# Kernel tuning notes

Hardware: AMD Instinct MI355X
Metric: run time of the kernel (lower is better)

Reference implementation:

```python
import jax, jax.numpy as jnp
import numpy as np

B, S, H, NH = 2, 2048, 1024, 16
HD = H // NH  # 64


def setup_inputs() -> dict:
    key = jax.random.key(0)
    ks = jax.random.split(key, 9)
    w = lambda k: jax.random.normal(k, (H, H), dtype=jnp.float32) * 0.02  # torch Linear weight [out,in]
    b = lambda k: jax.random.normal(k, (H,), dtype=jnp.float32) * 0.02
    return {
        "hidden_states": jax.random.normal(ks[0], (B, S, H), dtype=jnp.float32),
        "Wq": w(ks[1]), "bq": b(ks[2]),
        "Wk": w(ks[3]), "bk": b(ks[4]),
        "Wv": w(ks[5]), "bv": b(ks[6]),
        "Wo": w(ks[7]), "bo": b(ks[8]),
    }


def reference(hidden_states, Wq, bq, Wk, bk, Wv, bv, Wo, bo):
    b, s, h = hidden_states.shape
    nh, hd = NH, h // NH

    def proj(W, bias):
        y = hidden_states @ W.T + bias  # torch Linear: x W^T + b
        return y.reshape(b, s, nh, hd).transpose(0, 2, 1, 3)  # [b, h, s, d]

    q = proj(Wq, bq)
    k = proj(Wk, bk)
    v = proj(Wv, bv)

    scale = jnp.sqrt(jnp.asarray(hd, dtype=q.dtype))
    scores = jnp.einsum("bhqd,bhkd->bhqk", q, k) / scale  # [b, h, s, s]
    pos = jnp.arange(s)
    causal = pos[:, None] < pos[None, :]  # True where masked (key after query)
    scores = jnp.where(causal[None, None], -jnp.inf, scores)
    attn = jax.nn.softmax(scores, axis=-1)
    out = jnp.einsum("bhqk,bhkd->bhqd", attn, v)
    out = out.transpose(0, 2, 1, 3).reshape(b, s, h)
    return out @ Wo.T + bo
```

## Files before the change

kernel.cpp:

```cpp
#include <hip/hip_runtime.h>
#include <stdint.h>

typedef __bf16 bf16;
typedef __attribute__((ext_vector_type(2))) __bf16 bf16x2;
typedef __attribute__((ext_vector_type(4))) __bf16 bf16x4;
typedef __attribute__((ext_vector_type(8))) __bf16 bf16x8;
typedef __attribute__((ext_vector_type(4))) float f32x4;
typedef __attribute__((ext_vector_type(4))) short s16x4;

#define B_  2
#define S_  2048
#define H_  1024
#define NH_ 16
#define HD_ 64

__device__ __forceinline__ void glds16(const bf16* g, bf16* l) {
  __builtin_amdgcn_global_load_lds(
      (const __attribute__((address_space(1))) uint32_t*)g,
      (__attribute__((address_space(3))) uint32_t*)l, 16, 0, 0);
}

__device__ __forceinline__ f32x4 pv_mfma(bf16x4 a, bf16x4 b, f32x4 c) {
#if __has_builtin(__builtin_amdgcn_mfma_f32_16x16x16bf16_1k)
  union U { bf16x4 h; s16x4 s; };
  U ua; ua.h = a;
  U ub; ub.h = b;
  return __builtin_amdgcn_mfma_f32_16x16x16bf16_1k(ua.s, ub.s, c, 0, 0, 0);
#else
  f32x4 d;
  asm volatile("v_mfma_f32_16x16x16_bf16 %0, %1, %2, %3\n\ts_nop 7\n\ts_nop 7"
               : "=v"(d) : "v"(a), "v"(b), "v"(c));
  return d;
#endif
}

__global__ __launch_bounds__(256) void cvt_f32_bf16(
    const float* __restrict__ s0, bf16* __restrict__ d0, int n0,
    const float* __restrict__ s1, bf16* __restrict__ d1,
    const float* __restrict__ s2, bf16* __restrict__ d2,
    const float* __restrict__ s3, bf16* __restrict__ d3,
    const float* __restrict__ s4, bf16* __restrict__ d4, int nw)
{
  const float* s; bf16* d; int n;
  switch (blockIdx.y) {
    case 0:  s = s0; d = d0; n = n0; break;
    case 1:  s = s1; d = d1; n = nw; break;
    case 2:  s = s2; d = d2; n = nw; break;
    case 3:  s = s3; d = d3; n = nw; break;
    default: s = s4; d = d4; n = nw; break;
  }
  const int i = (blockIdx.x * 256 + threadIdx.x) * 8;
  if (i >= n) return;
  float4 v0 = *(const float4*)(s + i);
  float4 v1 = *(const float4*)(s + i + 4);
  bf16x8 o;
  o[0] = (bf16)v0.x; o[1] = (bf16)v0.y; o[2] = (bf16)v0.z; o[3] = (bf16)v0.w;
  o[4] = (bf16)v1.x; o[5] = (bf16)v1.y; o[6] = (bf16)v1.z; o[7] = (bf16)v1.w;
  *(bf16x8*)(d + i) = o;
}

__global__ __launch_bounds__(256) void gemm_qkv(
    const bf16* __restrict__ X,
    const bf16* __restrict__ W0, const bf16* __restrict__ W1, const bf16* __restrict__ W2,
    const float* __restrict__ b0, const float* __restrict__ b1, const float* __restrict__ b2,
    bf16* __restrict__ Y0, bf16* __restrict__ Y1, bf16* __restrict__ Y2,
    float ys0, int M, int N, int K)
{
  const bf16* W; const float* bias; bf16* Y; float ysc;
  if (blockIdx.z == 0)      { W = W0; bias = b0; Y = Y0; ysc = ys0; }
  else if (blockIdx.z == 1) { W = W1; bias = b1; Y = Y1; ysc = 1.0f; }
  else                      { W = W2; bias = b2; Y = Y2; ysc = 1.0f; }

  __shared__ __align__(16) bf16 As[2][128 * 32];
  __shared__ __align__(16) bf16 Bs[2][128 * 32];

  const int tid  = threadIdx.x;
  const int lane = tid & 63;
  const int wave = tid >> 6;
  const int m0 = blockIdx.y * 128;
  const int n0 = blockIdx.x * 128;
  const int wm = (wave >> 1) * 64;
  const int wn = (wave & 1) * 64;

  const int r0 = tid >> 2,            c0 = (tid & 3) * 8;
  const int r1 = (256 + tid) >> 2,    c1 = ((256 + tid) & 3) * 8;
  const int cb0 = (wave * 64) * 8;
  const int cb1 = (256 + wave * 64) * 8;

  f32x4 acc[4][4] = {};

  glds16(X + (size_t)(m0 + r0) * K + c0, &As[0][cb0]);
  glds16(W + (size_t)(n0 + r0) * K + c0, &Bs[0][cb0]);
  glds16(X + (size_t)(m0 + r1) * K + c1, &As[0][cb1]);
  glds16(W + (size_t)(n0 + r1) * K + c1, &Bs[0][cb1]);

  int pb = 0;
  for (int k0 = 0; k0 < K; k0 += 32, pb ^= 1) {
    __syncthreads();

    if (k0 + 32 < K) {
      const int kn = k0 + 32;
      glds16(X + (size_t)(m0 + r0) * K + kn + c0, &As[pb ^ 1][cb0]);
      glds16(W + (size_t)(n0 + r0) * K + kn + c0, &Bs[pb ^ 1][cb0]);
      glds16(X + (size_t)(m0 + r1) * K + kn + c1, &As[pb ^ 1][cb1]);
      glds16(W + (size_t)(n0 + r1) * K + kn + c1, &Bs[pb ^ 1][cb1]);
    }

    bf16x8 a[4], b[4];
#pragma unroll
    for (int i = 0; i < 4; ++i)
      a[i] = *(const bf16x8*)&As[pb][(wm + i * 16 + (lane & 15)) * 32 + (lane >> 4) * 8];
#pragma unroll
    for (int i = 0; i < 4; ++i)
      b[i] = *(const bf16x8*)&Bs[pb][(wn + i * 16 + (lane & 15)) * 32 + (lane >> 4) * 8];
#pragma unroll
    for (int mi = 0; mi < 4; ++mi)
#pragma unroll
      for (int ni = 0; ni < 4; ++ni)
        acc[mi][ni] = __builtin_amdgcn_mfma_f32_16x16x32_bf16(a[mi], b[ni], acc[mi][ni], 0, 0, 0);
  }

#pragma unroll
  for (int mi = 0; mi < 4; ++mi) {
    const int row = m0 + wm + mi * 16 + (lane >> 4) * 4;
#pragma unroll
    for (int ni = 0; ni < 4; ++ni) {
      const int col = n0 + wn + ni * 16 + (lane & 15);
      const float bv = bias[col];
#pragma unroll
      for (int r = 0; r < 4; ++r)
        Y[(size_t)(row + r) * N + col] = (bf16)((acc[mi][ni][r] + bv) * ysc);
    }
  }
}

__global__ __launch_bounds__(256) void gemm_o_64(
    const bf16* __restrict__ X, const bf16* __restrict__ W,
    const float* __restrict__ bias, float* __restrict__ Y)
{
  constexpr int K = 1024, N = 1024;
  __shared__ __align__(16) bf16 As[2][64 * 32];
  __shared__ __align__(16) bf16 Bs[2][128 * 32];

  const int tid  = threadIdx.x;
  const int lane = tid & 63;
  const int wave = tid >> 6;
  const int m0 = blockIdx.y * 64;
  const int n0 = blockIdx.x * 128;
  const int wm = (wave >> 1) * 32;
  const int wn = (wave & 1) * 64;

  const int ar = tid >> 2,  ac = (tid & 3) * 8;
  const int br0 = tid >> 2,          bc0 = (tid & 3) * 8;
  const int br1 = (256 + tid) >> 2,  bc1 = ((256 + tid) & 3) * 8;
  const int acb  = (wave * 64) * 8;
  const int bcb0 = (wave * 64) * 8;
  const int bcb1 = (256 + wave * 64) * 8;

  f32x4 acc[2][4] = {};

  glds16(X + (size_t)(m0 + ar) * K + ac,   &As[0][acb]);
  glds16(W + (size_t)(n0 + br0) * K + bc0, &Bs[0][bcb0]);
  glds16(W + (size_t)(n0 + br1) * K + bc1, &Bs[0][bcb1]);

  int pb = 0;
  for (int k0 = 0; k0 < K; k0 += 32, pb ^= 1) {
    __syncthreads();

    if (k0 + 32 < K) {
      const int kn = k0 + 32;
      glds16(X + (size_t)(m0 + ar) * K + kn + ac,   &As[pb ^ 1][acb]);
      glds16(W + (size_t)(n0 + br0) * K + kn + bc0, &Bs[pb ^ 1][bcb0]);
      glds16(W + (size_t)(n0 + br1) * K + kn + bc1, &Bs[pb ^ 1][bcb1]);
    }

    bf16x8 a[2], b[4];
#pragma unroll
    for (int i = 0; i < 2; ++i)
      a[i] = *(const bf16x8*)&As[pb][(wm + i * 16 + (lane & 15)) * 32 + (lane >> 4) * 8];
#pragma unroll
    for (int i = 0; i < 4; ++i)
      b[i] = *(const bf16x8*)&Bs[pb][(wn + i * 16 + (lane & 15)) * 32 + (lane >> 4) * 8];
#pragma unroll
    for (int mi = 0; mi < 2; ++mi)
#pragma unroll
      for (int ni = 0; ni < 4; ++ni)
        acc[mi][ni] = __builtin_amdgcn_mfma_f32_16x16x32_bf16(a[mi], b[ni], acc[mi][ni], 0, 0, 0);
  }

#pragma unroll
  for (int mi = 0; mi < 2; ++mi) {
    const int row = m0 + wm + mi * 16 + (lane >> 4) * 4;
#pragma unroll
    for (int ni = 0; ni < 4; ++ni) {
      const int col = n0 + wn + ni * 16 + (lane & 15);
      const float bv = bias[col];
#pragma unroll
      for (int r = 0; r < 4; ++r)
        Y[(size_t)(row + r) * N + col] = acc[mi][ni][r] + bv;
    }
  }
}


#define STAGE_K(k0_, buf_)                                                  \
  {                                                                         \
    _Pragma("unroll")                                                       \
    for (int j = 0; j < 4; ++j) {                                           \
      const int n = j * 256 + tid;                                          \
      const int row = n >> 3;                                               \
      const int cg  = (n & 7) ^ (row & 7);                                  \
      glds16(Kp + (size_t)((k0_) + row) * H_ + cg * 8,                      \
             &Ks[buf_][(j * 256 + wave * 64) * 8]);                         \
    }                                                                       \
  }

#define LOAD_V(k0_)                                                         \
  {                                                                         \
    vreg[0] = *(const bf16x8*)(Vp + (size_t)((k0_) + vr) * H_ + vc);        \
    vreg[1] = *(const bf16x8*)(Vp + (size_t)((k0_) + vr) * H_ + vc + 8);    \
    vreg[2] = *(const bf16x8*)(Vp + (size_t)((k0_) + vr + 1) * H_ + vc);    \
    vreg[3] = *(const bf16x8*)(Vp + (size_t)((k0_) + vr + 1) * H_ + vc + 8);\
  }

#define WRITE_V(buf_)                                                       \
  {                                                                         \
    _Pragma("unroll")                                                       \
    for (int e = 0; e < 8; ++e) {                                           \
      const int sw = (((vr >> 2) ^ e) * 4) + (vr & 3);                      \
      bf16x2 p0; p0[0] = vreg[0][e]; p0[1] = vreg[2][e];                    \
      *(bf16x2*)&Vt[buf_][(vc + e) * 128 + sw] = p0;                        \
      bf16x2 p1; p1[0] = vreg[1][e]; p1[1] = vreg[3][e];                    \
      *(bf16x2*)&Vt[buf_][(vc + 8 + e) * 128 + sw] = p1;                    \
    }                                                                       \
  }

#define SMAX(sacc, pwv, mr, lr, mxout, qrow_, last_)                        \
  {                                                                         \
    if (last_) {                                                            \
      _Pragma("unroll")                                                     \
      for (int mb = 0; mb < 8; ++mb) {                                      \
        const int kb = it * 128 + mb * 16 + quad * 4;                       \
        _Pragma("unroll")                                                   \
        for (int r = 0; r < 4; ++r)                                         \
          if (kb + r > (qrow_)) sacc[mb][r] = -1e30f;                       \
      }                                                                     \
    }                                                                       \
    float mx = -1e30f;                                                      \
    _Pragma("unroll")                                                       \
    for (int mb = 0; mb < 8; ++mb)                                          \
      mx = fmaxf(mx, fmaxf(fmaxf(sacc[mb][0], sacc[mb][1]),                 \
                           fmaxf(sacc[mb][2], sacc[mb][3])));               \
    mx = fmaxf(mx, __shfl_xor(mx, 16, 64));                                 \
    mx = fmaxf(mx, __shfl_xor(mx, 32, 64));                                 \
    (mxout) = mx;                                                           \
    float sum = 0.0f;                                                       \
    _Pragma("unroll")                                                       \
    for (int mb = 0; mb < 8; ++mb) {                                        \
      bf16x4 pw;                                                            \
      _Pragma("unroll")                                                     \
      for (int r = 0; r < 4; ++r) {                                         \
        const float p = __builtin_amdgcn_exp2f(sacc[mb][r] - (mr));         \
        sum += p;                                                           \
        pw[r] = (bf16)p;                                                    \
      }                                                                     \
      pwv[mb] = pw;                                                         \
    }                                                                       \
    sum += __shfl_xor(sum, 16, 64);                                         \
    sum += __shfl_xor(sum, 32, 64);                                         \
    (lr) += sum;                                                            \
  }

#define FIXUP(mx, mr, lr, oacc)                                             \
  if (!__all((mx) <= (mr) + 8.0f)) {                                        \
    const float mnew  = fmaxf((mr), (mx));                                  \
    const float alpha = __builtin_amdgcn_exp2f((mr) - mnew);                \
    (lr) *= alpha;                                                          \
    _Pragma("unroll")                                                       \
    for (int db = 0; db < 4; ++db)                                          \
      _Pragma("unroll")                                                     \
      for (int r = 0; r < 4; ++r) oacc[db][r] *= alpha;                     \
    (mr) = mnew;                                                            \
  }

#define ATTN_PROLOGUE()                                                     \
  const int lin  = blockIdx.x;                                              \
  const int slot = lin >> 3;                                                \
  const int bh   = (lin & 7) * 4 + (slot >> 4);                             \
  const int pair = slot & 15;                                               \
  const int b    = bh >> 4;                                                 \
  const int h    = bh & 15;                                                 \
  const int tid  = threadIdx.x;                                             \
  const int lane = tid & 63;                                                \
  const int wave = tid >> 6;                                                \
  const int quad = lane >> 4;                                               \
  const int l15  = lane & 15;                                               \
  const size_t headoff = (size_t)b * S_ * H_ + (size_t)h * HD_;             \
  const bf16* Kp = K + headoff;                                             \
  const bf16* Vp = V + headoff;                                             \
  const int qlo = pair, qhi = 31 - pair;                                    \
  const int nl  = (qlo >> 1) + 1;                                           \
  const int nh  = (qhi >> 1) + 1;                                           \
  const int qrowL = qlo * 64 + wave * 16 + l15;                             \
  const int qrowH = qhi * 64 + wave * 16 + l15;                             \
  bf16x8 bqL[2], bqH[2];                                                    \
  bqL[0] = *(const bf16x8*)(Q + headoff + (size_t)qrowL * H_ + quad * 8);   \
  bqL[1] = *(const bf16x8*)(Q + headoff + (size_t)qrowL * H_ + 32 + quad * 8); \
  bqH[0] = *(const bf16x8*)(Q + headoff + (size_t)qrowH * H_ + quad * 8);   \
  bqH[1] = *(const bf16x8*)(Q + headoff + (size_t)qrowH * H_ + 32 + quad * 8); \
  const int vr = lane * 2;                                                  \
  const int vc = wave * 16;                                                 \
  bf16x8 vreg[4];

#define ATTN_EPILOGUE()                                                     \
  const float invL = 1.0f / lrL;                                            \
  _Pragma("unroll")                                                         \
  for (int db = 0; db < 4; ++db) {                                          \
    bf16x4 o;                                                               \
    _Pragma("unroll")                                                       \
    for (int r = 0; r < 4; ++r) o[r] = (bf16)(oL[db][r] * invL);            \
    *(bf16x4*)(O + headoff + (size_t)qrowL * H_ + db * 16 + quad * 4) = o;  \
  }                                                                         \
  const float invH = 1.0f / lrH;                                            \
  _Pragma("unroll")                                                         \
  for (int db = 0; db < 4; ++db) {                                          \
    bf16x4 o;                                                               \
    _Pragma("unroll")                                                       \
    for (int r = 0; r < 4; ++r) o[r] = (bf16)(oH[db][r] * invH);            \
    *(bf16x4*)(O + headoff + (size_t)qrowH * H_ + db * 16 + quad * 4) = o;  \
  }

__device__ __forceinline__ void attn_tile_step(
    const bf16* Ksb, const bf16* Vtb, const bf16x8 bq[2], int qrow, int k0,
    bool maskit, float& mr, float& lr, f32x4 oacc[4], int l15, int quad)
{
  f32x4 sacc[8] = {};
  __builtin_amdgcn_s_setprio(1);
#pragma unroll
  for (int ks = 0; ks < 2; ++ks) {
#pragma unroll
    for (int mb = 0; mb < 8; ++mb) {
      const int row = mb * 16 + l15;
      const int ch  = (ks * 4 + quad) ^ (l15 & 7);
      bf16x8 ak = *(const bf16x8*)&Ksb[row * 64 + ch * 8];
      sacc[mb] = __builtin_amdgcn_mfma_f32_16x16x32_bf16(ak, bq[ks], sacc[mb], 0, 0, 0);
    }
  }
  __builtin_amdgcn_s_setprio(0);

  if (maskit) {
#pragma unroll
    for (int mb = 0; mb < 8; ++mb) {
      const int kb = k0 + mb * 16 + quad * 4;
#pragma unroll
      for (int r = 0; r < 4; ++r)
        if (kb + r > qrow) sacc[mb][r] = -1e30f;
    }
  }

  float mx = -1e30f;
#pragma unroll
  for (int mb = 0; mb < 8; ++mb)
    mx = fmaxf(mx, fmaxf(fmaxf(sacc[mb][0], sacc[mb][1]),
                         fmaxf(sacc[mb][2], sacc[mb][3])));
  mx = fmaxf(mx, __shfl_xor(mx, 16, 64));
  mx = fmaxf(mx, __shfl_xor(mx, 32, 64));

  float sum = 0.0f;
  bf16x4 pwv[8];
#pragma unroll
  for (int mb = 0; mb < 8; ++mb) {
    bf16x4 pw;
#pragma unroll
    for (int r = 0; r < 4; ++r) {
      const float p = __builtin_amdgcn_exp2f(sacc[mb][r] - mr);
      sum += p;
      pw[r] = (bf16)p;
    }
    pwv[mb] = pw;
  }
  sum += __shfl_xor(sum, 16, 64);
  sum += __shfl_xor(sum, 32, 64);

  __builtin_amdgcn_s_setprio(1);
#pragma unroll
  for (int mb = 0; mb < 8; ++mb) {
#pragma unroll
    for (int db = 0; db < 4; ++db) {
      const int vch = ((mb * 4 + quad) ^ (l15 & 7)) * 4;
      bf16x4 av = *(const bf16x4*)&Vtb[(db * 16 + l15) * 128 + vch];
      oacc[db] = pv_mfma(av, pwv[mb], oacc[db]);
    }
  }
  __builtin_amdgcn_s_setprio(0);

  lr += sum;
  if (!__all(mx <= mr + 8.0f)) {
    const float mnew  = fmaxf(mr, mx);
    const float alpha = __builtin_amdgcn_exp2f(mr - mnew);
    lr *= alpha;
#pragma unroll
    for (int db = 0; db < 4; ++db)
#pragma unroll
      for (int r = 0; r < 4; ++r) oacc[db][r] *= alpha;
    mr = mnew;
  }
}

__global__ __launch_bounds__(256, 2) void attn_fused(
    const bf16* __restrict__ Q, const bf16* __restrict__ K,
    const bf16* __restrict__ V, bf16* __restrict__ O)
{
  __shared__ __align__(16) bf16 Ks[2][128 * 64];
  __shared__ __align__(16) bf16 Vt[2][64 * 128];

  ATTN_PROLOGUE();

  STAGE_K(0, 0);
  LOAD_V(0);
  WRITE_V(0);
  __syncthreads();

  float mrL = 0.0f, lrL = 0.0f, mrH = 0.0f, lrH = 0.0f;
  f32x4 oL[4] = {}, oH[4] = {};

  for (int it = 0; it < nl; ++it) {
    const int c = it & 1;

    STAGE_K((it + 1) * 128, c ^ 1);
    LOAD_V((it + 1) * 128);

    f32x4 sH[8] = {}, sL[8] = {};
    __builtin_amdgcn_s_setprio(1);
#pragma unroll
    for (int ks = 0; ks < 2; ++ks) {
#pragma unroll
      for (int mb = 0; mb < 8; ++mb) {
        const int row = mb * 16 + l15;
        const int ch  = (ks * 4 + quad) ^ (l15 & 7);
        bf16x8 ak = *(const bf16x8*)&Ks[c][row * 64 + ch * 8];
        sH[mb] = __builtin_amdgcn_mfma_f32_16x16x32_bf16(ak, bqH[ks], sH[mb], 0, 0, 0);
        sL[mb] = __builtin_amdgcn_mfma_f32_16x16x32_bf16(ak, bqL[ks], sL[mb], 0, 0, 0);
      }
    }
    __builtin_amdgcn_s_setprio(0);

    bf16x4 pwH[8], pwL[8];
    float mxH = -1e30f, mxL = -1e30f;
    SMAX(sH, pwH, mrH, lrH, mxH, qrowH, false);
    SMAX(sL, pwL, mrL, lrL, mxL, qrowL, it == nl - 1);

    __builtin_amdgcn_s_setprio(1);
#pragma unroll
    for (int mb = 0; mb < 8; ++mb) {
#pragma unroll
      for (int db = 0; db < 4; ++db) {
        const int vch = ((mb * 4 + quad) ^ (l15 & 7)) * 4;
        bf16x4 av = *(const bf16x4*)&Vt[c][(db * 16 + l15) * 128 + vch];
        oH[db] = pv_mfma(av, pwH[mb], oH[db]);
        oL[db] = pv_mfma(av, pwL[mb], oL[db]);
      }
    }
    __builtin_amdgcn_s_setprio(0);

    FIXUP(mxH, mrH, lrH, oH);
    FIXUP(mxL, mrL, lrL, oL);

    WRITE_V(c ^ 1);
    __syncthreads();
  }

  for (int it = nl; it < nh; ++it) {
    const int c = it & 1;
    const bool pre = (it + 1 < nh);

    if (pre) {
      STAGE_K((it + 1) * 128, c ^ 1);
      LOAD_V((it + 1) * 128);
    }

    attn_tile_step(Ks[c], Vt[c], bqH, qrowH, it * 128, it == nh - 1,
                   mrH, lrH, oH, l15, quad);

    if (pre) {
      WRITE_V(c ^ 1);
      __syncthreads();
    }
  }

  ATTN_EPILOGUE();
}

__global__ __launch_bounds__(256, 2) void attn_safe(
    const bf16* __restrict__ Q, const bf16* __restrict__ K,
    const bf16* __restrict__ V, bf16* __restrict__ O)
{
  __shared__ __align__(16) bf16 Ks[2][128 * 64];
  __shared__ __align__(16) bf16 Vt[2][64 * 128];

  ATTN_PROLOGUE();

  STAGE_K(0, 0);
  LOAD_V(0);
  WRITE_V(0);
  __syncthreads();

  float mrL = 0.0f, lrL = 0.0f, mrH = 0.0f, lrH = 0.0f;
  f32x4 oL[4] = {}, oH[4] = {};

  for (int it = 0; it < nh; ++it) {
    const int c = it & 1;
    const bool pre = (it + 1 < nh);

    if (pre) {
      STAGE_K((it + 1) * 128, c ^ 1);
      LOAD_V((it + 1) * 128);
    }

    attn_tile_step(Ks[c], Vt[c], bqH, qrowH, it * 128, it == nh - 1,
                   mrH, lrH, oH, l15, quad);
    if (it < nl)
      attn_tile_step(Ks[c], Vt[c], bqL, qrowL, it * 128, it == nl - 1,
                     mrL, lrL, oL, l15, quad);

    if (pre) {
      WRITE_V(c ^ 1);
      __syncthreads();
    }
  }

  ATTN_EPILOGUE();
}

extern "C" void kernel_launch(void* const* d_in, const int* in_sizes, int n_in,
                              void* d_out, int out_size, void* d_ws, size_t ws_size,
                              hipStream_t stream) {
  const float* hs = (const float*)d_in[0];
  const float* Wq = (const float*)d_in[1]; const float* bq = (const float*)d_in[2];
  const float* Wk = (const float*)d_in[3]; const float* bk = (const float*)d_in[4];
  const float* Wv = (const float*)d_in[5]; const float* bv = (const float*)d_in[6];
  const float* Wo = (const float*)d_in[7]; const float* bo = (const float*)d_in[8];
  float* out = (float*)d_out;

  const size_t elems = (size_t)B_ * S_ * H_;
  const size_t wel   = (size_t)H_ * H_;
  bf16* hsb = (bf16*)d_ws;
  bf16* AO  = hsb;
  bf16* Wqb = hsb + elems;
  bf16* Wkb = Wqb + wel;
  bf16* Wvb = Wkb + wel;
  bf16* Wob = Wvb + wel;
  bf16* Qw  = Wob + wel;
  bf16* Kw  = Qw + elems;
  bf16* Vw  = Kw + elems;

  static int use_fused = -1;
  if (use_fused < 0) {
    hipFuncAttributes fa;
    if (hipFuncGetAttributes(&fa, (const void*)attn_fused) == hipSuccess &&
        fa.localSizeBytes == 0 && fa.numRegs <= 256)
      use_fused = 1;
    else
      use_fused = 0;
  }

  cvt_f32_bf16<<<dim3(2048, 5), dim3(256), 0, stream>>>(
      hs, hsb, (int)elems, Wq, Wqb, Wk, Wkb, Wv, Wvb, Wo, Wob, (int)wel);

  const int M = B_ * S_;
  const float QSCL = 0.125f * 1.44269504f;

  gemm_qkv<<<dim3(H_ / 128, M / 128, 3), dim3(256), 0, stream>>>(
      hsb, Wqb, Wkb, Wvb, bq, bk, bv, Qw, Kw, Vw, QSCL, M, H_, H_);

  if (use_fused)
    attn_fused<<<dim3(512), dim3(256), 0, stream>>>(Qw, Kw, Vw, AO);
  else
    attn_safe<<<dim3(512), dim3(256), 0, stream>>>(Qw, Kw, Vw, AO);

  gemm_o_64<<<dim3(8, 64), dim3(256), 0, stream>>>(AO, Wob, bo, out);
}
```

Measured before the change: 198.2 us.

## Add 256-key-tile attention kernel with 8 waves split across paired query tiles

Adds a new attention kernel, launched with 512 threads per block and double-buffered 256-key K/V tiles in LDS. Waves 0-3 handle the high query tile and waves 4-7 the low query tile, so each staged K/V tile is shared by both tiles' waves instead of one set of waves looping over both. The aim is fewer staging iterations and barriers and more MFMA work per tile. In exchange, each block uses about 128KB of LDS, which likely limits a CU to one block, and the low-tile waves sit idle through barriers once their causal range ends. The old safe fallback is removed, and the previous fused kernel becomes the fallback.

```diff
diff --git a/kernel.cpp b/kernel.cpp
--- a/kernel.cpp
+++ b/kernel.cpp
@@ -283,52 +283,189 @@
     (mr) = mnew;                                                            \
   }
 
-#define ATTN_PROLOGUE()                                                     \
-  const int lin  = blockIdx.x;                                              \
-  const int slot = lin >> 3;                                                \
-  const int bh   = (lin & 7) * 4 + (slot >> 4);                             \
-  const int pair = slot & 15;                                               \
-  const int b    = bh >> 4;                                                 \
-  const int h    = bh & 15;                                                 \
-  const int tid  = threadIdx.x;                                             \
-  const int lane = tid & 63;                                                \
-  const int wave = tid >> 6;                                                \
-  const int quad = lane >> 4;                                               \
-  const int l15  = lane & 15;                                               \
-  const size_t headoff = (size_t)b * S_ * H_ + (size_t)h * HD_;             \
-  const bf16* Kp = K + headoff;                                             \
-  const bf16* Vp = V + headoff;                                             \
-  const int qlo = pair, qhi = 31 - pair;                                    \
-  const int nl  = (qlo >> 1) + 1;                                           \
-  const int nh  = (qhi >> 1) + 1;                                           \
-  const int qrowL = qlo * 64 + wave * 16 + l15;                             \
-  const int qrowH = qhi * 64 + wave * 16 + l15;                             \
-  bf16x8 bqL[2], bqH[2];                                                    \
-  bqL[0] = *(const bf16x8*)(Q + headoff + (size_t)qrowL * H_ + quad * 8);   \
-  bqL[1] = *(const bf16x8*)(Q + headoff + (size_t)qrowL * H_ + 32 + quad * 8); \
-  bqH[0] = *(const bf16x8*)(Q + headoff + (size_t)qrowH * H_ + quad * 8);   \
-  bqH[1] = *(const bf16x8*)(Q + headoff + (size_t)qrowH * H_ + 32 + quad * 8); \
-  const int vr = lane * 2;                                                  \
-  const int vc = wave * 16;                                                 \
+__global__ __launch_bounds__(512, 2) void attn_k256(
+    const bf16* __restrict__ Q, const bf16* __restrict__ K,
+    const bf16* __restrict__ V, bf16* __restrict__ O)
+{
+  const int lin  = blockIdx.x;
+  const int slot = lin >> 3;
+  const int bh   = (lin & 7) * 4 + (slot >> 4);
+  const int pair = slot & 15;
+  const int b    = bh >> 4;
+  const int h    = bh & 15;
+
+  const int tid  = threadIdx.x;
+  const int lane = tid & 63;
+  const int wave = tid >> 6;
+  const int quad = lane >> 4;
+  const int l15  = lane & 15;
+  const size_t headoff = (size_t)b * S_ * H_ + (size_t)h * HD_;
+  const bf16* Kp = K + headoff;
+  const bf16* Vp = V + headoff;
+
+  __shared__ __align__(16) bf16 Ks[2][256 * 64];
+  __shared__ __align__(16) bf16 Vt[2][64 * 256];
+
+  const int qlo = pair, qhi = 31 - pair;
+  const int nhp = (35 - pair) >> 2;
+  const int nlp = (pair + 4) >> 2;
+  const bool isH = wave < 4;
+  const int  myq = isH ? qhi : qlo;
+  const int  myn = isH ? nhp : nlp;
+  const int qrow = myq * 64 + (wave & 3) * 16 + l15;
+
+  bf16x8 bq[2];
+  bq[0] = *(const bf16x8*)(Q + headoff + (size_t)qrow * H_ + quad * 8);
+  bq[1] = *(const bf16x8*)(Q + headoff + (size_t)qrow * H_ + 32 + quad * 8);
+
+  const int kp = tid & 127;
+  const int g  = tid >> 7;
+  const int vr = kp * 2;
+  const int vc = g * 16;
+
+#define STAGE_K2(k0_, buf_)                                                 \
+  {                                                                         \
+    _Pragma("unroll")                                                       \
+    for (int j = 0; j < 4; ++j) {                                           \
+      const int n = j * 512 + tid;                                          \
+      const int row = n >> 3;                                               \
+      const int cg  = (n & 7) ^ (row & 7);                                  \
+      glds16(Kp + (size_t)((k0_) + row) * H_ + cg * 8,                      \
+             &Ks[buf_][(j * 512 + wave * 64) * 8]);                         \
+    }                                                                       \
+  }
+
+#define LOAD_V2(k0_)                                                        \
+  {                                                                         \
+    vreg[0] = *(const bf16x8*)(Vp + (size_t)((k0_) + vr) * H_ + vc);        \
+    vreg[1] = *(const bf16x8*)(Vp + (size_t)((k0_) + vr) * H_ + vc + 8);    \
+    vreg[2] = *(const bf16x8*)(Vp + (size_t)((k0_) + vr + 1) * H_ + vc);    \
+    vreg[3] = *(const bf16x8*)(Vp + (size_t)((k0_) + vr + 1) * H_ + vc + 8);\
+  }
+
+#define WRITE_V2(buf_)                                                      \
+  {                                                                         \
+    _Pragma("unroll")                                                       \
+    for (int e = 0; e < 8; ++e) {                                           \
+      const int sw = (((vr >> 2) ^ e) * 4) + (vr & 3);                      \
+      bf16x2 p0; p0[0] = vreg[0][e]; p0[1] = vreg[2][e];                    \
+      *(bf16x2*)&Vt[buf_][(vc + e) * 256 + sw] = p0;                        \
+      bf16x2 p1; p1[0] = vreg[1][e]; p1[1] = vreg[3][e];                    \
+      *(bf16x2*)&Vt[buf_][(vc + 8 + e) * 256 + sw] = p1;                    \
+    }                                                                       \
+  }
+
   bf16x8 vreg[4];
 
-#define ATTN_EPILOGUE()                                                     \
-  const float invL = 1.0f / lrL;                                            \
-  _Pragma("unroll")                                                         \
-  for (int db = 0; db < 4; ++db) {                                          \
-    bf16x4 o;                                                               \
-    _Pragma("unroll")                                                       \
-    for (int r = 0; r < 4; ++r) o[r] = (bf16)(oL[db][r] * invL);            \
-    *(bf16x4*)(O + headoff + (size_t)qrowL * H_ + db * 16 + quad * 4) = o;  \
-  }                                                                         \
-  const float invH = 1.0f / lrH;                                            \
-  _Pragma("unroll")                                                         \
-  for (int db = 0; db < 4; ++db) {                                          \
-    bf16x4 o;                                                               \
-    _Pragma("unroll")                                                       \
-    for (int r = 0; r < 4; ++r) o[r] = (bf16)(oH[db][r] * invH);            \
-    *(bf16x4*)(O + headoff + (size_t)qrowH * H_ + db * 16 + quad * 4) = o;  \
-  }
+  STAGE_K2(0, 0);
+  LOAD_V2(0);
+  WRITE_V2(0);
+  __syncthreads();
+
+  float mr = 0.0f, lr = 0.0f;
+  f32x4 oacc[4] = {};
+
+  for (int it = 0; it < nhp; ++it) {
+    const int c = it & 1;
+    const bool pre = (it + 1 < nhp);
+
+    if (pre) {
+      STAGE_K2((it + 1) * 256, c ^ 1);
+      LOAD_V2((it + 1) * 256);
+    }
+
+    if (it < myn) {
+      f32x4 sacc[16] = {};
+      __builtin_amdgcn_s_setprio(1);
+#pragma unroll
+      for (int ks = 0; ks < 2; ++ks) {
+#pragma unroll
+        for (int mb = 0; mb < 16; ++mb) {
+          const int row = mb * 16 + l15;
+          const int ch  = (ks * 4 + quad) ^ (l15 & 7);
+          bf16x8 ak = *(const bf16x8*)&Ks[c][row * 64 + ch * 8];
+          sacc[mb] = __builtin_amdgcn_mfma_f32_16x16x32_bf16(ak, bq[ks], sacc[mb], 0, 0, 0);
+        }
+      }
+      __builtin_amdgcn_s_setprio(0);
+
+      if (it == myn - 1) {
+#pragma unroll
+        for (int mb = 0; mb < 16; ++mb) {
+          const int kb = it * 256 + mb * 16 + quad * 4;
+#pragma unroll
+          for (int r = 0; r < 4; ++r)
+            if (kb + r > qrow) sacc[mb][r] = -1e30f;
+        }
+      }
+
+      float mx = -1e30f;
+#pragma unroll
+      for (int mb = 0; mb < 16; ++mb)
+        mx = fmaxf(mx, fmaxf(fmaxf(sacc[mb][0], sacc[mb][1]),
+                             fmaxf(sacc[mb][2], sacc[mb][3])));
+      mx = fmaxf(mx, __shfl_xor(mx, 16, 64));
+      mx = fmaxf(mx, __shfl_xor(mx, 32, 64));
+
+      float sum = 0.0f;
+      bf16x4 pwv[16];
+#pragma unroll
+      for (int mb = 0; mb < 16; ++mb) {
+        bf16x4 pw;
+#pragma unroll
+        for (int r = 0; r < 4; ++r) {
+          const float p = __builtin_amdgcn_exp2f(sacc[mb][r] - mr);
+          sum += p;
+          pw[r] = (bf16)p;
+        }
+        pwv[mb] = pw;
+      }
+      sum += __shfl_xor(sum, 16, 64);
+      sum += __shfl_xor(sum, 32, 64);
+      lr += sum;
+
+      __builtin_amdgcn_s_setprio(1);
+#pragma unroll
+      for (int mb = 0; mb < 16; ++mb) {
+#pragma unroll
+        for (int db = 0; db < 4; ++db) {
+          const int vch = ((mb * 4 + quad) ^ (l15 & 7)) * 4;
+          bf16x4 av = *(const bf16x4*)&Vt[c][(db * 16 + l15) * 256 + vch];
+          oacc[db] = pv_mfma(av, pwv[mb], oacc[db]);
+        }
+      }
+      __builtin_amdgcn_s_setprio(0);
+
+      if (!__all(mx <= mr + 8.0f)) {
+        const float mnew  = fmaxf(mr, mx);
+        const float alpha = __builtin_amdgcn_exp2f(mr - mnew);
+        lr *= alpha;
+#pragma unroll
+        for (int db = 0; db < 4; ++db)
+#pragma unroll
+          for (int r = 0; r < 4; ++r) oacc[db][r] *= alpha;
+        mr = mnew;
+      }
+    }
+
+    if (pre) {
+      WRITE_V2(c ^ 1);
+      __syncthreads();
+    }
+  }
+
+  const float inv = 1.0f / lr;
+#pragma unroll
+  for (int db = 0; db < 4; ++db) {
+    bf16x4 o;
+#pragma unroll
+    for (int r = 0; r < 4; ++r) o[r] = (bf16)(oacc[db][r] * inv);
+    *(bf16x4*)(O + headoff + (size_t)qrow * H_ + db * 16 + quad * 4) = o;
+  }
+#undef STAGE_K2
+#undef LOAD_V2
+#undef WRITE_V2
+}
 
 __device__ __forceinline__ void attn_tile_step(
     const bf16* Ksb, const bf16* Vtb, const bf16x8 bq[2], int qrow, int k0,
@@ -414,7 +551,33 @@
   __shared__ __align__(16) bf16 Ks[2][128 * 64];
   __shared__ __align__(16) bf16 Vt[2][64 * 128];
 
-  ATTN_PROLOGUE();
+  const int lin  = blockIdx.x;
+  const int slot = lin >> 3;
+  const int bh   = (lin & 7) * 4 + (slot >> 4);
+  const int pair = slot & 15;
+  const int b    = bh >> 4;
+  const int h    = bh & 15;
+  const int tid  = threadIdx.x;
+  const int lane = tid & 63;
+  const int wave = tid >> 6;
+  const int quad = lane >> 4;
+  const int l15  = lane & 15;
+  const size_t headoff = (size_t)b * S_ * H_ + (size_t)h * HD_;
+  const bf16* Kp = K + headoff;
+  const bf16* Vp = V + headoff;
+  const int qlo = pair, qhi = 31 - pair;
+  const int nl  = (qlo >> 1) + 1;
+  const int nh  = (qhi >> 1) + 1;
+  const int qrowL = qlo * 64 + wave * 16 + l15;
+  const int qrowH = qhi * 64 + wave * 16 + l15;
+  bf16x8 bqL[2], bqH[2];
+  bqL[0] = *(const bf16x8*)(Q + headoff + (size_t)qrowL * H_ + quad * 8);
+  bqL[1] = *(const bf16x8*)(Q + headoff + (size_t)qrowL * H_ + 32 + quad * 8);
+  bqH[0] = *(const bf16x8*)(Q + headoff + (size_t)qrowH * H_ + quad * 8);
+  bqH[1] = *(const bf16x8*)(Q + headoff + (size_t)qrowH * H_ + 32 + quad * 8);
+  const int vr = lane * 2;
+  const int vc = wave * 16;
+  bf16x8 vreg[4];
 
   STAGE_K(0, 0);
   LOAD_V(0);
@@ -488,48 +651,22 @@
     }
   }
 
-  ATTN_EPILOGUE();
-}
-
-__global__ __launch_bounds__(256, 2) void attn_safe(
-    const bf16* __restrict__ Q, const bf16* __restrict__ K,
-    const bf16* __restrict__ V, bf16* __restrict__ O)
-{
-  __shared__ __align__(16) bf16 Ks[2][128 * 64];
-  __shared__ __align__(16) bf16 Vt[2][64 * 128];
-
-  ATTN_PROLOGUE();
-
-  STAGE_K(0, 0);
-  LOAD_V(0);
-  WRITE_V(0);
-  __syncthreads();
-
-  float mrL = 0.0f, lrL = 0.0f, mrH = 0.0f, lrH = 0.0f;
-  f32x4 oL[4] = {}, oH[4] = {};
-
-  for (int it = 0; it < nh; ++it) {
-    const int c = it & 1;
-    const bool pre = (it + 1 < nh);
-
-    if (pre) {
-      STAGE_K((it + 1) * 128, c ^ 1);
-      LOAD_V((it + 1) * 128);
-    }
-
-    attn_tile_step(Ks[c], Vt[c], bqH, qrowH, it * 128, it == nh - 1,
-                   mrH, lrH, oH, l15, quad);
-    if (it < nl)
-      attn_tile_step(Ks[c], Vt[c], bqL, qrowL, it * 128, it == nl - 1,
-                     mrL, lrL, oL, l15, quad);
-
-    if (pre) {
-      WRITE_V(c ^ 1);
-      __syncthreads();
-    }
-  }
-
-  ATTN_EPILOGUE();
+  const float invL = 1.0f / lrL;
+#pragma unroll
+  for (int db = 0; db < 4; ++db) {
+    bf16x4 o;
+#pragma unroll
+    for (int r = 0; r < 4; ++r) o[r] = (bf16)(oL[db][r] * invL);
+    *(bf16x4*)(O + headoff + (size_t)qrowL * H_ + db * 16 + quad * 4) = o;
+  }
+  const float invH = 1.0f / lrH;
+#pragma unroll
+  for (int db = 0; db < 4; ++db) {
+    bf16x4 o;
+#pragma unroll
+    for (int r = 0; r < 4; ++r) o[r] = (bf16)(oH[db][r] * invH);
+    *(bf16x4*)(O + headoff + (size_t)qrowH * H_ + db * 16 + quad * 4) = o;
+  }
 }
 
 extern "C" void kernel_launch(void* const* d_in, const int* in_sizes, int n_in,
@@ -554,14 +691,14 @@
   bf16* Kw  = Qw + elems;
   bf16* Vw  = Kw + elems;
 
-  static int use_fused = -1;
-  if (use_fused < 0) {
+  static int use_k256 = -1;
+  if (use_k256 < 0) {
     hipFuncAttributes fa;
-    if (hipFuncGetAttributes(&fa, (const void*)attn_fused) == hipSuccess &&
+    if (hipFuncGetAttributes(&fa, (const void*)attn_k256) == hipSuccess &&
         fa.localSizeBytes == 0 && fa.numRegs <= 256)
-      use_fused = 1;
+      use_k256 = 1;
     else
-      use_fused = 0;
+      use_k256 = 0;
   }
 
   cvt_f32_bf16<<<dim3(2048, 5), dim3(256), 0, stream>>>(
@@ -573,10 +710,10 @@
   gemm_qkv<<<dim3(H_ / 128, M / 128, 3), dim3(256), 0, stream>>>(
       hsb, Wqb, Wkb, Wvb, bq, bk, bv, Qw, Kw, Vw, QSCL, M, H_, H_);
 
-  if (use_fused)
+  if (use_k256)
+    attn_k256<<<dim3(512), dim3(512), 0, stream>>>(Qw, Kw, Vw, AO);
+  else
     attn_fused<<<dim3(512), dim3(256), 0, stream>>>(Qw, Kw, Vw, AO);
-  else
-    attn_safe<<<dim3(512), dim3(256), 0, stream>>>(Qw, Kw, Vw, AO);
 
   gemm_o_64<<<dim3(8, 64), dim3(256), 0, stream>>>(AO, Wob, bo, out);
 }
```

Measured after the change: 215.9 us. 1.09x slower.
